# Optimization experiments

Measured on AMD Instinct MI355X. Metric: run time of the kernel, lower is better.

The kernel has to match this reference:

```python
import jax, jax.numpy as jnp
import numpy as np

DENSE_W = 0.7  # unused in learned fusion path but kept for parity
SPARSE_W = 0.3

def _l2norm(x):
    return x / jnp.linalg.norm(x, axis=-1, keepdims=True)

def setup_inputs() -> dict:
    key = jax.random.key(0)
    ks = jax.random.split(key, 8)
    Q, D, dim = 32, 4096, 384
    feat = 2 * dim + 2  # 770
    query_dense = _l2norm(jax.random.normal(ks[0], (Q, dim), jnp.float32))
    doc_dense = _l2norm(jax.random.normal(ks[1], (D, dim), jnp.float32))
    sparse_scores = jax.random.uniform(ks[2], (Q, D), jnp.float32)
    W1 = jax.random.normal(ks[3], (feat, 384), jnp.float32) * (1.0 / np.sqrt(feat))
    b1 = jnp.zeros((384,), jnp.float32)
    W2 = jax.random.normal(ks[4], (384, 192), jnp.float32) * (1.0 / np.sqrt(384))
    b2 = jnp.zeros((192,), jnp.float32)
    W3 = jax.random.normal(ks[5], (192, 1), jnp.float32) * (1.0 / np.sqrt(192))
    b3 = jnp.zeros((1,), jnp.float32)
    return {"query_dense": query_dense, "doc_dense": doc_dense,
            "sparse_scores": sparse_scores,
            "W1": W1, "b1": b1, "W2": W2, "b2": b2, "W3": W3, "b3": b3}

def reference(query_dense, doc_dense, sparse_scores, W1, b1, W2, b2, W3, b3):
    # dense cosine similarity (inputs are L2-normalized): [Q, D]
    dense_scores = query_dense @ doc_dense.T
    Q, D = dense_scores.shape
    dim = query_dense.shape[1]
    # Vectorized equivalent of the per-pair gather+concat double loop:
    # feature[q, d] = [query_dense[q], doc_dense[d], dense[q,d], sparse[q,d]]
    qf = jnp.broadcast_to(query_dense[:, None, :], (Q, D, dim))
    df = jnp.broadcast_to(doc_dense[None, :, :], (Q, D, dim))
    features = jnp.concatenate(
        [qf, df, dense_scores[..., None], sparse_scores[..., None]], axis=-1)  # [Q, D, 2*dim+2]
    # 4-layer fusion MLP (Dropout is identity at inference)
    h = jax.nn.relu(features @ W1 + b1)
    h = jax.nn.relu(h @ W2 + b2)
    fusion_weights = jax.nn.sigmoid((h @ W3 + b3)[..., 0])  # [Q, D]
    final_scores = fusion_weights * dense_scores + (1.0 - fusion_weights) * sparse_scores
    return final_scores, dense_scores, sparse_scores
```

## Files before the change

### kernel.cpp

```cpp
#include <hip/hip_runtime.h>
#include <hip/hip_bf16.h>

typedef __attribute__((ext_vector_type(2)))  float f32x2;
typedef __attribute__((ext_vector_type(4)))  float f32x4;
typedef __attribute__((ext_vector_type(8)))  short bf16x8;
typedef __attribute__((ext_vector_type(2)))  unsigned int u32x2;
typedef __attribute__((ext_vector_type(4)))  unsigned int u32x4;

__device__ __forceinline__ short f2bf(float x){
    __hip_bfloat16 h = __float2bfloat16(x);
    return __builtin_bit_cast(short, h);
}
__device__ __forceinline__ float bf2f(short x){
    unsigned int u = ((unsigned int)(unsigned short)x) << 16;
    return __builtin_bit_cast(float, u);
}
__device__ __forceinline__ unsigned int cvt2(float lo, float hi){
    unsigned int r;
    asm("v_cvt_pk_bf16_f32 %0, %1, %2" : "=v"(r) : "v"(lo), "v"(hi));
    return r;
}

__global__ __launch_bounds__(256)
void pre0_kernel(const float* __restrict__ query, const float* __restrict__ doc,
                 const float* __restrict__ W1, const float* __restrict__ W2,
                 short* __restrict__ W1t, short* __restrict__ docb, short* __restrict__ qb16,
                 float* __restrict__ W1cdf, short* __restrict__ W2t){
    const int b = blockIdx.x, tid = threadIdx.x;

    if (b < 72){
        const int lt0 = b*256 + tid;
        #pragma unroll
        for (int i=0;i<2;i++){
            const int lt    = lt0 + i*18432;
            const int chunk = lt >> 6, lane = lt & 63;
            const int cl = lane & 15, quad = lane >> 4;
            const int half = (chunk >= 288) ? 1 : 0;
            const int cs = chunk - half*288;
            const int s = cs/24, ct = cs%24;
            const float* src = W1 + (half*384 + s*32 + quad*8)*384 + ct*16 + cl;
            float v[8];
            #pragma unroll
            for (int j=0;j<8;j++) v[j] = src[j*384];
            u32x4 o;
            o[0] = cvt2(v[0],v[1]); o[1] = cvt2(v[2],v[3]);
            o[2] = cvt2(v[4],v[5]); o[3] = cvt2(v[6],v[7]);
            *(u32x4*)(W1t + chunk*512 + lane*8) = o;
        }
    } else if (b < 168){
        const int t0 = (b-72)*256 + tid;
        #pragma unroll
        for (int i=0;i<16;i++){
            const int g = t0 + i*24576;
            const f32x4 v = *(const f32x4*)(doc + g*4);
            u32x2 o; o[0] = cvt2(v[0],v[1]); o[1] = cvt2(v[2],v[3]);
            *(u32x2*)(docb + g*4) = o;
        }
    } else if (b == 168){
        #pragma unroll
        for (int i=0;i<12;i++){
            const int g = tid + i*256;
            const f32x4 v = *(const f32x4*)(query + g*4);
            u32x2 o; o[0] = cvt2(v[0],v[1]); o[1] = cvt2(v[2],v[3]);
            *(u32x2*)(qb16 + g*4) = o;
        }
    } else if (b == 169){
        #pragma unroll
        for (int i=0;i<3;i++){
            int o = tid + i*256;
            W1cdf[o] = (o < 384) ? W1[768*384 + o] : W1[769*384 + (o - 384)];
        }
    } else {
        const int t0 = (b - 170)*256 + tid;
        #pragma unroll
        for (int i=0;i<9;i++){
            int c = t0 + i*1024;
            int lane_c = c & 63, st = c >> 6;
            int s = st/12, t2 = st%12;
            int n = t2*16 + (lane_c&15), kb = s*32 + ((lane_c>>4)&3)*8;
            bf16x8 v;
            #pragma unroll
            for (int j=0;j<8;j++) v[j] = f2bf(W2[(kb+j)*192 + n]);
            *(bf16x8*)(W2t + c*8) = v;
        }
    }
}

__global__ __launch_bounds__(256)
void pre1_kernel(const short* __restrict__ docb, const short* __restrict__ qb16,
                 const short* __restrict__ W1t, const float* __restrict__ b1,
                 const float* __restrict__ sparse,
                 short* __restrict__ Bws, float* __restrict__ Aq,
                 float* __restrict__ out_dense, float* __restrict__ out_sparse){
    const int b = blockIdx.x, tid = threadIdx.x;
    const int w = tid >> 6, lane = tid & 63;
    const int cl = lane & 15, quad = lane >> 4;

    const short* src; const short* wt; int r0; bool isA;
    if (b < 256){ r0 = b*16;       src = docb; wt = W1t + 147456; isA = false; }
    else        { r0 = (b-256)*16; src = qb16; wt = W1t;          isA = true;  }

    const int tq = w & 1;
    const short* ap = src + (r0+cl)*384 + quad*8;
    const short* wp = wt + (w*6)*512 + lane*8;
    const short* qp = qb16 + (tq*16 + cl)*384 + quad*8;

    f32x4 acc[6];
    #pragma unroll
    for (int t=0;t<6;t++) acc[t] = (f32x4){0.f,0.f,0.f,0.f};
    f32x4 accd = (f32x4){0.f,0.f,0.f,0.f};

    bf16x8 a_c = *(const bf16x8*)(ap);
    bf16x8 qd_c = *(const bf16x8*)(qp);
    bf16x8 b_c[6];
    #pragma unroll
    for (int tt=0;tt<6;tt++) b_c[tt] = *(const bf16x8*)(wp + tt*512);

    #pragma unroll 1
    for (int s=0;s<12;s++){
        const int sn = (s < 11) ? s+1 : 0;
        const bf16x8 a_n  = *(const bf16x8*)(ap + sn*32);
        const bf16x8 qd_n = *(const bf16x8*)(qp + sn*32);
        bf16x8 b_n[6];
        #pragma unroll
        for (int tt=0;tt<6;tt++) b_n[tt] = *(const bf16x8*)(wp + sn*12288 + tt*512);
        #pragma unroll
        for (int tt=0;tt<6;tt++)
            acc[tt] = __builtin_amdgcn_mfma_f32_16x16x32_bf16(a_c, b_c[tt], acc[tt], 0, 0, 0);
        accd = __builtin_amdgcn_mfma_f32_16x16x32_bf16(a_c, qd_c, accd, 0, 0, 0);
        a_c = a_n; qd_c = qd_n;
        #pragma unroll
        for (int tt=0;tt<6;tt++) b_c[tt] = b_n[tt];
    }

    #pragma unroll
    for (int tt=0;tt<6;tt++){
        const int col = (w*6+tt)*16 + cl;
        if (isA){
            const float b1v = b1[col];
            #pragma unroll
            for (int r=0;r<4;r++)
                Aq[(r0 + quad*4 + r)*384 + col] = acc[tt][r] + b1v;
        } else {
            #pragma unroll
            for (int r=0;r<4;r++)
                Bws[(r0 + quad*4 + r)*384 + col] = f2bf(acc[tt][r]);
        }
    }
    if (!isA){
        if (w < 2){
            #pragma unroll
            for (int r=0;r<4;r++)
                out_dense[(tq*16 + cl)*4096 + r0 + quad*4 + r] = accd[r];
        }
        if (tid < 128){
            const int qq = tid>>2, c4 = tid&3;
            *(f32x4*)(out_sparse + qq*4096 + r0 + c4*4) =
                *(const f32x4*)(sparse + qq*4096 + r0 + c4*4);
        }
    }
}

__global__ __launch_bounds__(1024)
void main_kernel(const float* __restrict__ Aq, const short* __restrict__ Bws,
                 const float* __restrict__ W1cdf, const short* __restrict__ W2t,
                 const float* __restrict__ b2, const float* __restrict__ W3,
                 const float* __restrict__ b3, const float* __restrict__ sparse,
                 const float* __restrict__ dense_in, float* __restrict__ out_final){
    __shared__ __align__(16) short lw[73728];
    __shared__ __align__(16) float lcd[768];
    const int tid = threadIdx.x;

    #pragma unroll
    for (int i=0;i<9;i++){
        int c = tid + i*1024;
        *(f32x4*)(lw + c*8) = *(const f32x4*)(W2t + c*8);
    }
    if (tid < 192)
        *(f32x4*)(lcd + tid*4) = *(const f32x4*)(W1cdf + tid*4);
    __syncthreads();

    const int lane = tid & 63, w = tid >> 6;
    const int colslot = w >> 1, mhalf = w & 1;
    const int cl = lane & 15, g = lane >> 4;
    const int mrow = mhalf*16 + cl;
    const int k8 = g*8;
    const float b3v = b3[0];
    const int dcol0 = blockIdx.x*16 + colslot;

    #pragma unroll 1
    for (int t4=0; t4<2; t4++){
        const int dcol = dcol0 + t4*8;
        const float dsv = dense_in[mrow*4096 + dcol];
        const float ssv = sparse[mrow*4096 + dcol];
        const f32x2 dsv2 = {dsv, dsv}, ssv2 = {ssv, ssv};

        f32x4 acc[12];
        #pragma unroll
        for (int t=0;t<12;t++) acc[t] = (f32x4){0.f,0.f,0.f,0.f};

        const short* bp = Bws + dcol*384;
        const float* ap = Aq + mrow*384;

        bf16x8 bwC = *(const bf16x8*)(bp + k8);
        f32x4  aC0 = *(const f32x4*)(ap + k8);
        f32x4  aC1 = *(const f32x4*)(ap + k8 + 4);

        #pragma unroll 1
        for (int s=0; s<12; s++){
            const int kn = (s < 11) ? (s+1)*32 + k8 : k8;
            const bf16x8 bwN = *(const bf16x8*)(bp + kn);
            const f32x4  aN0 = *(const f32x4*)(ap + kn);
            const f32x4  aN1 = *(const f32x4*)(ap + kn + 4);

            const int kf = s*32 + k8;
            const f32x4 wcA = *(const f32x4*)(lcd + kf);
            const f32x4 wcB = *(const f32x4*)(lcd + kf + 4);
            const f32x4 wdA = *(const f32x4*)(lcd + 384 + kf);
            const f32x4 wdB = *(const f32x4*)(lcd + 384 + kf + 4);

            u32x4 frw;
            { f32x2 h = {aC0[0] + bf2f(bwC[0]), aC0[1] + bf2f(bwC[1])};
              h += dsv2 * (f32x2){wcA[0],wcA[1]}; h += ssv2 * (f32x2){wdA[0],wdA[1]};
              frw[0] = cvt2(fmaxf(h[0],0.f), fmaxf(h[1],0.f)); }
            { f32x2 h = {aC0[2] + bf2f(bwC[2]), aC0[3] + bf2f(bwC[3])};
              h += dsv2 * (f32x2){wcA[2],wcA[3]}; h += ssv2 * (f32x2){wdA[2],wdA[3]};
              frw[1] = cvt2(fmaxf(h[0],0.f), fmaxf(h[1],0.f)); }
            { f32x2 h = {aC1[0] + bf2f(bwC[4]), aC1[1] + bf2f(bwC[5])};
              h += dsv2 * (f32x2){wcB[0],wcB[1]}; h += ssv2 * (f32x2){wdB[0],wdB[1]};
              frw[2] = cvt2(fmaxf(h[0],0.f), fmaxf(h[1],0.f)); }
            { f32x2 h = {aC1[2] + bf2f(bwC[6]), aC1[3] + bf2f(bwC[7])};
              h += dsv2 * (f32x2){wcB[2],wcB[3]}; h += ssv2 * (f32x2){wdB[2],wdB[3]};
              frw[3] = cvt2(fmaxf(h[0],0.f), fmaxf(h[1],0.f)); }
            const bf16x8 fr = __builtin_bit_cast(bf16x8, frw);

            const short* lp = lw + s*6144 + lane*8;
            #pragma unroll
            for (int tg=0; tg<4; tg++){
                const bf16x8 f0 = *(const bf16x8*)(lp + (tg*3+0)*512);
                const bf16x8 f1 = *(const bf16x8*)(lp + (tg*3+1)*512);
                const bf16x8 f2 = *(const bf16x8*)(lp + (tg*3+2)*512);
                acc[tg*3+0] = __builtin_amdgcn_mfma_f32_16x16x32_bf16(fr, f0, acc[tg*3+0], 0, 0, 0);
                acc[tg*3+1] = __builtin_amdgcn_mfma_f32_16x16x32_bf16(fr, f1, acc[tg*3+1], 0, 0, 0);
                acc[tg*3+2] = __builtin_amdgcn_mfma_f32_16x16x32_bf16(fr, f2, acc[tg*3+2], 0, 0, 0);
            }
            bwC = bwN; aC0 = aN0; aC1 = aN1;
        }

        float p0=0.f, p1=0.f, p2=0.f, p3=0.f;
        #pragma unroll
        for (int t=0;t<12;t++){
            const int n = t*16 + cl;
            const float b2v = b2[n];
            const float w3v = W3[n];
            p0 += fmaxf(acc[t][0] + b2v, 0.0f) * w3v;
            p1 += fmaxf(acc[t][1] + b2v, 0.0f) * w3v;
            p2 += fmaxf(acc[t][2] + b2v, 0.0f) * w3v;
            p3 += fmaxf(acc[t][3] + b2v, 0.0f) * w3v;
        }
        #pragma unroll
        for (int mask=1; mask<16; mask<<=1){
            p0 += __shfl_xor(p0, mask);
            p1 += __shfl_xor(p1, mask);
            p2 += __shfl_xor(p2, mask);
            p3 += __shfl_xor(p3, mask);
        }
        float myp = p0;
        myp = (cl==1) ? p1 : myp;
        myp = (cl==2) ? p2 : myp;
        myp = (cl==3) ? p3 : myp;
        if (cl < 4){
            const int row = mhalf*16 + g*4 + cl;
            const float logit = myp + b3v;
            const float wgt = 1.0f/(1.0f + __expf(-logit));
            const float dd = dense_in[row*4096 + dcol];
            const float ss = sparse[row*4096 + dcol];
            out_final[row*4096 + dcol] = wgt*dd + (1.0f - wgt)*ss;
        }
    }
}

extern "C" void kernel_launch(void* const* d_in, const int* in_sizes, int n_in,
                              void* d_out, int out_size, void* d_ws, size_t ws_size,
                              hipStream_t stream){
    const float* query  = (const float*)d_in[0];
    const float* doc    = (const float*)d_in[1];
    const float* sparse = (const float*)d_in[2];
    const float* W1     = (const float*)d_in[3];
    const float* b1     = (const float*)d_in[4];
    const float* W2     = (const float*)d_in[5];
    const float* b2     = (const float*)d_in[6];
    const float* W3     = (const float*)d_in[7];
    const float* b3     = (const float*)d_in[8];

    float* out_final  = (float*)d_out;
    float* out_dense  = (float*)d_out + 131072;
    float* out_sparse = (float*)d_out + 262144;

    short* Bws   = (short*)d_ws;
    float* Aq    = (float*)((char*)d_ws + 3145728);
    float* W1cdf = (float*)((char*)d_ws + 3194880);
    short* W2t   = (short*)((char*)d_ws + 3197952);
    short* W1t   = (short*)((char*)d_ws + 3345408);
    short* docb  = (short*)((char*)d_ws + 3935232);
    short* qb16  = (short*)((char*)d_ws + 7080960);

    hipLaunchKernelGGL(pre0_kernel, dim3(174), dim3(256), 0, stream,
                       query, doc, W1, W2, W1t, docb, qb16, W1cdf, W2t);
    hipLaunchKernelGGL(pre1_kernel, dim3(258), dim3(256), 0, stream,
                       docb, qb16, W1t, b1, sparse, Bws, Aq, out_dense, out_sparse);
    hipLaunchKernelGGL(main_kernel, dim3(256), dim3(1024), 0, stream,
                       Aq, Bws, W1cdf, W2t, b2, W3, b3, sparse, out_dense, out_final);
}
```

Measured before the change: 123.4 us.

## Fuse doc-side projection and dense scores into main kernel, drop a launch

```diff
diff --git a/kernel.cpp b/kernel.cpp
--- a/kernel.cpp
+++ b/kernel.cpp
@@ -22,10 +22,10 @@
 }
 
 __global__ __launch_bounds__(256)
-void pre0_kernel(const float* __restrict__ query, const float* __restrict__ doc,
-                 const float* __restrict__ W1, const float* __restrict__ W2,
-                 short* __restrict__ W1t, short* __restrict__ docb, short* __restrict__ qb16,
-                 float* __restrict__ W1cdf, short* __restrict__ W2t){
+void prep_kernel(const float* __restrict__ query, const float* __restrict__ W1,
+                 const float* __restrict__ b1, const float* __restrict__ W2,
+                 short* __restrict__ W1t, float* __restrict__ W1cdf,
+                 short* __restrict__ W2t, float* __restrict__ Aq){
     const int b = blockIdx.x, tid = threadIdx.x;
 
     if (b < 72){
@@ -47,31 +47,8 @@
             o[2] = cvt2(v[4],v[5]); o[3] = cvt2(v[6],v[7]);
             *(u32x4*)(W1t + chunk*512 + lane*8) = o;
         }
-    } else if (b < 168){
-        const int t0 = (b-72)*256 + tid;
-        #pragma unroll
-        for (int i=0;i<16;i++){
-            const int g = t0 + i*24576;
-            const f32x4 v = *(const f32x4*)(doc + g*4);
-            u32x2 o; o[0] = cvt2(v[0],v[1]); o[1] = cvt2(v[2],v[3]);
-            *(u32x2*)(docb + g*4) = o;
-        }
-    } else if (b == 168){
-        #pragma unroll
-        for (int i=0;i<12;i++){
-            const int g = tid + i*256;
-            const f32x4 v = *(const f32x4*)(query + g*4);
-            u32x2 o; o[0] = cvt2(v[0],v[1]); o[1] = cvt2(v[2],v[3]);
-            *(u32x2*)(qb16 + g*4) = o;
-        }
-    } else if (b == 169){
-        #pragma unroll
-        for (int i=0;i<3;i++){
-            int o = tid + i*256;
-            W1cdf[o] = (o < 384) ? W1[768*384 + o] : W1[769*384 + (o - 384)];
-        }
-    } else {
-        const int t0 = (b - 170)*256 + tid;
+    } else if (b < 76){
+        const int t0 = (b - 72)*256 + tid;
         #pragma unroll
         for (int i=0;i<9;i++){
             int c = t0 + i*1024;
@@ -83,115 +60,154 @@
             for (int j=0;j<8;j++) v[j] = f2bf(W2[(kb+j)*192 + n]);
             *(bf16x8*)(W2t + c*8) = v;
         }
-    }
-}
-
-__global__ __launch_bounds__(256)
-void pre1_kernel(const short* __restrict__ docb, const short* __restrict__ qb16,
-                 const short* __restrict__ W1t, const float* __restrict__ b1,
-                 const float* __restrict__ sparse,
-                 short* __restrict__ Bws, float* __restrict__ Aq,
-                 float* __restrict__ out_dense, float* __restrict__ out_sparse){
-    const int b = blockIdx.x, tid = threadIdx.x;
-    const int w = tid >> 6, lane = tid & 63;
-    const int cl = lane & 15, quad = lane >> 4;
-
-    const short* src; const short* wt; int r0; bool isA;
-    if (b < 256){ r0 = b*16;       src = docb; wt = W1t + 147456; isA = false; }
-    else        { r0 = (b-256)*16; src = qb16; wt = W1t;          isA = true;  }
-
-    const int tq = w & 1;
-    const short* ap = src + (r0+cl)*384 + quad*8;
-    const short* wp = wt + (w*6)*512 + lane*8;
-    const short* qp = qb16 + (tq*16 + cl)*384 + quad*8;
-
-    f32x4 acc[6];
-    #pragma unroll
-    for (int t=0;t<6;t++) acc[t] = (f32x4){0.f,0.f,0.f,0.f};
-    f32x4 accd = (f32x4){0.f,0.f,0.f,0.f};
-
-    bf16x8 a_c = *(const bf16x8*)(ap);
-    bf16x8 qd_c = *(const bf16x8*)(qp);
-    bf16x8 b_c[6];
-    #pragma unroll
-    for (int tt=0;tt<6;tt++) b_c[tt] = *(const bf16x8*)(wp + tt*512);
-
-    #pragma unroll 1
-    for (int s=0;s<12;s++){
-        const int sn = (s < 11) ? s+1 : 0;
-        const bf16x8 a_n  = *(const bf16x8*)(ap + sn*32);
-        const bf16x8 qd_n = *(const bf16x8*)(qp + sn*32);
-        bf16x8 b_n[6];
-        #pragma unroll
-        for (int tt=0;tt<6;tt++) b_n[tt] = *(const bf16x8*)(wp + sn*12288 + tt*512);
-        #pragma unroll
-        for (int tt=0;tt<6;tt++)
-            acc[tt] = __builtin_amdgcn_mfma_f32_16x16x32_bf16(a_c, b_c[tt], acc[tt], 0, 0, 0);
-        accd = __builtin_amdgcn_mfma_f32_16x16x32_bf16(a_c, qd_c, accd, 0, 0, 0);
-        a_c = a_n; qd_c = qd_n;
-        #pragma unroll
-        for (int tt=0;tt<6;tt++) b_c[tt] = b_n[tt];
-    }
-
-    #pragma unroll
-    for (int tt=0;tt<6;tt++){
-        const int col = (w*6+tt)*16 + cl;
-        if (isA){
+    } else if (b == 76){
+        #pragma unroll
+        for (int i=0;i<3;i++){
+            int o = tid + i*256;
+            W1cdf[o] = (o < 384) ? W1[768*384 + o] : W1[769*384 + (o - 384)];
+        }
+    } else {
+        const int r0 = (b - 77)*16;
+        const int w = tid >> 6, lane = tid & 63;
+        const int cl = lane & 15, quad = lane >> 4;
+
+        f32x4 acc[6];
+        #pragma unroll
+        for (int t=0;t<6;t++) acc[t] = (f32x4){0.f,0.f,0.f,0.f};
+
+        #pragma unroll 1
+        for (int s=0;s<12;s++){
+            const float* ap = query + (r0+cl)*384 + s*32 + quad*8;
+            const f32x4 a0 = *(const f32x4*)ap;
+            const f32x4 a1 = *(const f32x4*)(ap+4);
+            u32x4 ua;
+            ua[0] = cvt2(a0[0],a0[1]); ua[1] = cvt2(a0[2],a0[3]);
+            ua[2] = cvt2(a1[0],a1[1]); ua[3] = cvt2(a1[2],a1[3]);
+            const bf16x8 af = __builtin_bit_cast(bf16x8, ua);
+            const float* wk = W1 + (s*32 + quad*8)*384;
+            #pragma unroll
+            for (int tt=0;tt<6;tt++){
+                const int col = (w*6+tt)*16 + cl;
+                bf16x8 bfv;
+                #pragma unroll
+                for (int j=0;j<8;j++) bfv[j] = f2bf(wk[j*384 + col]);
+                acc[tt] = __builtin_amdgcn_mfma_f32_16x16x32_bf16(af, bfv, acc[tt], 0, 0, 0);
+            }
+        }
+        #pragma unroll
+        for (int tt=0;tt<6;tt++){
+            const int col = (w*6+tt)*16 + cl;
             const float b1v = b1[col];
             #pragma unroll
             for (int r=0;r<4;r++)
                 Aq[(r0 + quad*4 + r)*384 + col] = acc[tt][r] + b1v;
-        } else {
-            #pragma unroll
-            for (int r=0;r<4;r++)
-                Bws[(r0 + quad*4 + r)*384 + col] = f2bf(acc[tt][r]);
         }
     }
-    if (!isA){
-        if (w < 2){
-            #pragma unroll
-            for (int r=0;r<4;r++)
-                out_dense[(tq*16 + cl)*4096 + r0 + quad*4 + r] = accd[r];
-        }
-        if (tid < 128){
-            const int qq = tid>>2, c4 = tid&3;
-            *(f32x4*)(out_sparse + qq*4096 + r0 + c4*4) =
-                *(const f32x4*)(sparse + qq*4096 + r0 + c4*4);
-        }
-    }
 }
 
 __global__ __launch_bounds__(1024)
-void main_kernel(const float* __restrict__ Aq, const short* __restrict__ Bws,
+void main_kernel(const float* __restrict__ doc, const float* __restrict__ query,
+                 const float* __restrict__ Aq, const short* __restrict__ W1t,
                  const float* __restrict__ W1cdf, const short* __restrict__ W2t,
                  const float* __restrict__ b2, const float* __restrict__ W3,
                  const float* __restrict__ b3, const float* __restrict__ sparse,
-                 const float* __restrict__ dense_in, float* __restrict__ out_final){
+                 float* __restrict__ out_dense, float* __restrict__ out_sparse,
+                 float* __restrict__ out_final){
     __shared__ __align__(16) short lw[73728];
+    __shared__ __align__(16) short lbw[6144];
     __shared__ __align__(16) float lcd[768];
-    const int tid = threadIdx.x;
-
-    #pragma unroll
-    for (int i=0;i<9;i++){
-        int c = tid + i*1024;
-        *(f32x4*)(lw + c*8) = *(const f32x4*)(W2t + c*8);
+    const int tid = threadIdx.x, bb = blockIdx.x;
+    const int r0 = bb*16;
+    const int lane = tid & 63, w = tid >> 6;
+
+    if (w < 4){
+        const int cl = lane & 15, quad = lane >> 4, tq = w & 1;
+        const float* ap = doc + (r0+cl)*384 + quad*8;
+        const float* qp = query + (tq*16 + cl)*384 + quad*8;
+        const short* wp = W1t + 147456 + (w*6)*512 + lane*8;
+
+        f32x4 acc[6];
+        #pragma unroll
+        for (int t=0;t<6;t++) acc[t] = (f32x4){0.f,0.f,0.f,0.f};
+        f32x4 accd = (f32x4){0.f,0.f,0.f,0.f};
+
+        f32x4 a0c = *(const f32x4*)(ap),  a1c = *(const f32x4*)(ap+4);
+        f32x4 q0c = *(const f32x4*)(qp),  q1c = *(const f32x4*)(qp+4);
+        bf16x8 b_c[6];
+        #pragma unroll
+        for (int tt=0;tt<6;tt++) b_c[tt] = *(const bf16x8*)(wp + tt*512);
+
+        #pragma unroll 1
+        for (int s=0;s<12;s++){
+            const int sn = (s < 11) ? s+1 : 0;
+            const f32x4 a0n = *(const f32x4*)(ap + sn*32);
+            const f32x4 a1n = *(const f32x4*)(ap + sn*32 + 4);
+            const f32x4 q0n = *(const f32x4*)(qp + sn*32);
+            const f32x4 q1n = *(const f32x4*)(qp + sn*32 + 4);
+            bf16x8 b_n[6];
+            #pragma unroll
+            for (int tt=0;tt<6;tt++) b_n[tt] = *(const bf16x8*)(wp + sn*12288 + tt*512);
+
+            u32x4 ua, uq;
+            ua[0] = cvt2(a0c[0],a0c[1]); ua[1] = cvt2(a0c[2],a0c[3]);
+            ua[2] = cvt2(a1c[0],a1c[1]); ua[3] = cvt2(a1c[2],a1c[3]);
+            uq[0] = cvt2(q0c[0],q0c[1]); uq[1] = cvt2(q0c[2],q0c[3]);
+            uq[2] = cvt2(q1c[0],q1c[1]); uq[3] = cvt2(q1c[2],q1c[3]);
+            const bf16x8 af = __builtin_bit_cast(bf16x8, ua);
+            const bf16x8 qf = __builtin_bit_cast(bf16x8, uq);
+
+            #pragma unroll
+            for (int tt=0;tt<6;tt++)
+                acc[tt] = __builtin_amdgcn_mfma_f32_16x16x32_bf16(af, b_c[tt], acc[tt], 0, 0, 0);
+            accd = __builtin_amdgcn_mfma_f32_16x16x32_bf16(af, qf, accd, 0, 0, 0);
+
+            a0c = a0n; a1c = a1n; q0c = q0n; q1c = q1n;
+            #pragma unroll
+            for (int tt=0;tt<6;tt++) b_c[tt] = b_n[tt];
+        }
+
+        #pragma unroll
+        for (int tt=0;tt<6;tt++){
+            const int col = (w*6+tt)*16 + cl;
+            #pragma unroll
+            for (int r=0;r<4;r++)
+                lbw[(quad*4 + r)*384 + col] = f2bf(acc[tt][r]);
+        }
+        if (w < 2){
+            #pragma unroll
+            for (int r=0;r<4;r++)
+                out_dense[(tq*16 + cl)*4096 + r0 + quad*4 + r] = accd[r];
+        }
+    } else {
+        #pragma unroll
+        for (int i=0;i<12;i++){
+            const int c = (w-4)*64 + lane + i*768;
+            *(f32x4*)(lw + c*8) = *(const f32x4*)(W2t + c*8);
+        }
+        if (tid >= 256 && tid < 448){
+            const int t = tid - 256;
+            *(f32x4*)(lcd + t*4) = *(const f32x4*)(W1cdf + t*4);
+        }
+        if (tid >= 512 && tid < 640){
+            const int idx = tid - 512;
+            const int qq = idx >> 2, c4 = idx & 3;
+            *(f32x4*)(out_sparse + qq*4096 + r0 + c4*4) =
+                *(const f32x4*)(sparse + qq*4096 + r0 + c4*4);
+        }
     }
-    if (tid < 192)
-        *(f32x4*)(lcd + tid*4) = *(const f32x4*)(W1cdf + tid*4);
     __syncthreads();
 
-    const int lane = tid & 63, w = tid >> 6;
     const int colslot = w >> 1, mhalf = w & 1;
     const int cl = lane & 15, g = lane >> 4;
     const int mrow = mhalf*16 + cl;
     const int k8 = g*8;
     const float b3v = b3[0];
-    const int dcol0 = blockIdx.x*16 + colslot;
+    const int dcol0 = r0 + colslot;
 
     #pragma unroll 1
     for (int t4=0; t4<2; t4++){
         const int dcol = dcol0 + t4*8;
-        const float dsv = dense_in[mrow*4096 + dcol];
+        const float dsv = out_dense[mrow*4096 + dcol];
         const float ssv = sparse[mrow*4096 + dcol];
         const f32x2 dsv2 = {dsv, dsv}, ssv2 = {ssv, ssv};
 
@@ -199,7 +215,7 @@
         #pragma unroll
         for (int t=0;t<12;t++) acc[t] = (f32x4){0.f,0.f,0.f,0.f};
 
-        const short* bp = Bws + dcol*384;
+        const short* bp = lbw + (dcol - r0)*384;
         const float* ap = Aq + mrow*384;
 
         bf16x8 bwC = *(const bf16x8*)(bp + k8);
@@ -273,7 +289,7 @@
             const int row = mhalf*16 + g*4 + cl;
             const float logit = myp + b3v;
             const float wgt = 1.0f/(1.0f + __expf(-logit));
-            const float dd = dense_in[row*4096 + dcol];
+            const float dd = out_dense[row*4096 + dcol];
             const float ss = sparse[row*4096 + dcol];
             out_final[row*4096 + dcol] = wgt*dd + (1.0f - wgt)*ss;
         }
@@ -297,18 +313,14 @@
     float* out_dense  = (float*)d_out + 131072;
     float* out_sparse = (float*)d_out + 262144;
 
-    short* Bws   = (short*)d_ws;
-    float* Aq    = (float*)((char*)d_ws + 3145728);
-    float* W1cdf = (float*)((char*)d_ws + 3194880);
-    short* W2t   = (short*)((char*)d_ws + 3197952);
-    short* W1t   = (short*)((char*)d_ws + 3345408);
-    short* docb  = (short*)((char*)d_ws + 3935232);
-    short* qb16  = (short*)((char*)d_ws + 7080960);
-
-    hipLaunchKernelGGL(pre0_kernel, dim3(174), dim3(256), 0, stream,
-                       query, doc, W1, W2, W1t, docb, qb16, W1cdf, W2t);
-    hipLaunchKernelGGL(pre1_kernel, dim3(258), dim3(256), 0, stream,
-                       docb, qb16, W1t, b1, sparse, Bws, Aq, out_dense, out_sparse);
+    short* W1t   = (short*)d_ws;
+    short* W2t   = (short*)((char*)d_ws + 589824);
+    float* W1cdf = (float*)((char*)d_ws + 737280);
+    float* Aq    = (float*)((char*)d_ws + 740352);
+
+    hipLaunchKernelGGL(prep_kernel, dim3(79), dim3(256), 0, stream,
+                       query, W1, b1, W2, W1t, W1cdf, W2t, Aq);
     hipLaunchKernelGGL(main_kernel, dim3(256), dim3(1024), 0, stream,
-                       Aq, Bws, W1cdf, W2t, b2, W3, b3, sparse, out_dense, out_final);
-}
+                       doc, query, Aq, W1t, W1cdf, W2t, b2, W3, b3, sparse,
+                       out_dense, out_sparse, out_final);
+}
```

Result: no change. 123.8 us (+0.4%).
